# Kernel tuning notes

Measured on AMD Instinct MI355X. Metric: run time of the kernel, lower is better.

Reference implementation:

```python
import jax, jax.numpy as jnp
import numpy as np

ROPE_BASE = 10000.0
NUM_HEADS = 16

def _rotate_half(x):
    d = x.shape[-1] // 2
    return jnp.concatenate([-x[..., d:], x[..., :d]], axis=-1)

def setup_inputs() -> dict:
    key = jax.random.key(0)
    ks = jax.random.split(key, 5)
    b, s, d = 1, 2048, 2048
    scale = 1.0 / np.sqrt(d)
    return {
        "hidden_states": jax.random.normal(ks[0], (b, s, d), jnp.float32),
        "wq": jax.random.normal(ks[1], (d, d), jnp.float32) * scale,
        "wk": jax.random.normal(ks[2], (d, d), jnp.float32) * scale,
        "wv": jax.random.normal(ks[3], (d, d), jnp.float32) * scale,
        "wo": jax.random.normal(ks[4], (d, d), jnp.float32) * scale,
        "position_ids": jnp.broadcast_to(jnp.arange(s, dtype=jnp.int32), (b, s)),
    }

def reference(hidden_states, wq, wk, wv, wo, position_ids):
    b, s, d = hidden_states.shape
    h = NUM_HEADS
    dh = d // h
    # q/k/v projections (torch Linear: y = x @ W^T), split heads -> bhsd
    def proj(w):
        return jnp.einsum('bsd,ed->bse', hidden_states, w).reshape(b, s, h, dh).transpose(0, 2, 1, 3)
    q, k, v = proj(wq), proj(wk), proj(wv)
    # rotary embedding (LLaMA style): freqs over half dim, duplicated
    inv_freq = 1.0 / (ROPE_BASE ** (jnp.arange(0, dh, 2, dtype=jnp.float32) / dh))
    t = jnp.arange(s, dtype=jnp.float32)
    freqs = jnp.einsum('s,f->sf', t, inv_freq)              # [s, dh/2]
    emb = jnp.concatenate([freqs, freqs], axis=-1)          # [s, dh]
    cos = jnp.cos(emb)[position_ids][:, None, :, :]         # [b,1,s,dh]
    sin = jnp.sin(emb)[position_ids][:, None, :, :]
    q = q * cos + _rotate_half(q) * sin
    k = k * cos + _rotate_half(k) * sin
    # full (non-causal) scaled dot-product attention, as in the SDPA fast path
    scores = jnp.einsum('bhqd,bhkd->bhqk', q, k) / jnp.sqrt(jnp.float32(dh))
    attn = jax.nn.softmax(scores, axis=-1)
    out = jnp.einsum('bhqk,bhkd->bhqd', attn, v)            # [b,h,s,dh]
    out = out.transpose(0, 2, 1, 3).reshape(b, s, d)
    return jnp.einsum('bsd,ed->bse', out, wo)
```

## Files before the change

### kernel.cpp

```cpp
#include <hip/hip_runtime.h>

typedef unsigned short ushort_t;
typedef unsigned int uint32;
typedef __attribute__((ext_vector_type(8))) short short8;
typedef __attribute__((ext_vector_type(4))) float f32x4;
typedef __attribute__((ext_vector_type(2))) uint32 u32x2;

#define LDS_LOAD16(gptr, lptr)                                                             \
  __builtin_amdgcn_global_load_lds((const __attribute__((address_space(1))) uint32*)(gptr),\
                                   (__attribute__((address_space(3))) uint32*)(lptr),      \
                                   16, 0, 0)

__device__ __forceinline__ ushort_t f2b(float f) {
  uint32 u = __builtin_bit_cast(uint32, f);
  u += 0x7fffu + ((u >> 16) & 1u);
  return (ushort_t)(u >> 16);
}
__device__ __forceinline__ uint32 pk2(float a, float b) {
  return (uint32)f2b(a) | ((uint32)f2b(b) << 16);
}
__device__ __forceinline__ int swz8(int r) { return (r ^ (r >> 3)) & 7; }

constexpr size_t E = (size_t)2048 * 2048;

__global__ __launch_bounds__(256) void k_cvt5(const float* __restrict__ a0, const float* __restrict__ a1,
                                              const float* __restrict__ a2, const float* __restrict__ a3,
                                              const float* __restrict__ a4, ushort_t* __restrict__ out) {
  const float* srcs[5] = {a0, a1, a2, a3, a4};
  const float* s = srcs[blockIdx.y];
  size_t i = ((size_t)blockIdx.x * 256 + threadIdx.x) * 4;
  float4 v = *(const float4*)(s + i);
  ushort4 o;
  o.x = f2b(v.x); o.y = f2b(v.y); o.z = f2b(v.z); o.w = f2b(v.w);
  *(ushort4*)(out + (size_t)blockIdx.y * E + i) = o;
}

__global__ __launch_bounds__(256) void k_gemm_qkv(const ushort_t* __restrict__ A,
                                                  const ushort_t* __restrict__ B0,
                                                  const ushort_t* __restrict__ B1,
                                                  const ushort_t* __restrict__ B2,
                                                  ushort_t* __restrict__ Qm,
                                                  ushort_t* __restrict__ Km,
                                                  ushort_t* __restrict__ Vt,
                                                  const int* __restrict__ pos) {
  __shared__ ushort_t As[128 * 64];
  __shared__ ushort_t Bs[128 * 64];
  const int tid = threadIdx.x;
  const int lane = tid & 63, wave = tid >> 6;
  const int quad = lane >> 4, l16 = lane & 15;
  const int wm = wave >> 1, wn = wave & 1;
  const int z = blockIdx.z;
  const ushort_t* Bp = (z == 0) ? B0 : (z == 1) ? B1 : B2;
  const size_t row0 = (size_t)blockIdx.y * 128, col0 = (size_t)blockIdx.x * 128;

  int g[4];
#pragma unroll
  for (int j = 0; j < 4; ++j) g[j] = (j & 1) + ((j >> 1) << 2) + wn * 2;

  f32x4 zero = {0.f, 0.f, 0.f, 0.f};
  f32x4 acc[4][4];
#pragma unroll
  for (int i = 0; i < 4; ++i)
#pragma unroll
    for (int j = 0; j < 4; ++j) acc[i][j] = zero;

  for (int kt = 0; kt < 32; ++kt) {
#pragma unroll
    for (int j2 = 0; j2 < 4; ++j2) {
      int c = tid + 256 * j2;
      int r = c >> 3, p = c & 7;
      int sc = (p ^ swz8(r)) * 8;
      LDS_LOAD16(A + (row0 + r) * 2048 + kt * 64 + sc, &As[c * 8]);
      LDS_LOAD16(Bp + (col0 + r) * 2048 + kt * 64 + sc, &Bs[c * 8]);
    }
    __syncthreads();
    short8 a[4][2], b[4][2];
#pragma unroll
    for (int i = 0; i < 4; ++i) {
      int ra = wm * 64 + i * 16 + l16;
#pragma unroll
      for (int kk = 0; kk < 2; ++kk)
        a[i][kk] = *(const short8*)&As[(ra * 8 + ((kk * 4 + quad) ^ swz8(ra))) * 8];
    }
#pragma unroll
    for (int j = 0; j < 4; ++j) {
      int rb = g[j] * 16 + l16;
#pragma unroll
      for (int kk = 0; kk < 2; ++kk)
        b[j][kk] = *(const short8*)&Bs[(rb * 8 + ((kk * 4 + quad) ^ swz8(rb))) * 8];
    }
#pragma unroll
    for (int kk = 0; kk < 2; ++kk)
#pragma unroll
      for (int i = 0; i < 4; ++i)
#pragma unroll
        for (int j = 0; j < 4; ++j)
          acc[i][j] = __builtin_amdgcn_mfma_f32_16x16x32_bf16(a[i][kk], b[j][kk], acc[i][j], 0, 0, 0);
    __syncthreads();
  }

  if (z < 2) {
    ushort_t* C = z ? Km : Qm;
    const float mul = z ? 1.0f : 0.08838834764831845f;
#pragma unroll
    for (int i = 0; i < 4; ++i)
#pragma unroll
      for (int r = 0; r < 4; ++r) {
        size_t row = row0 + wm * 64 + i * 16 + quad * 4 + r;
        float pt = (float)pos[row];
        size_t rowoff = row * 2048 + col0;
#pragma unroll
        for (int j = 0; j < 2; ++j) {
          int f = g[j] * 16 + l16;
          float ang = pt * __expf(-0.14391156831212787f * (float)f);
          float sn, cs;
          __sincosf(ang, &sn, &cs);
          cs *= mul; sn *= mul;
          float q0 = acc[i][j][r], q1 = acc[i][j + 2][r];
          C[rowoff + f]      = f2b(q0 * cs - q1 * sn);
          C[rowoff + f + 64] = f2b(q1 * cs + q0 * sn);
        }
      }
  } else {
#pragma unroll
    for (int i = 0; i < 4; ++i)
#pragma unroll
      for (int j = 0; j < 4; ++j) {
        size_t col = col0 + g[j] * 16 + l16;
        size_t rowb = row0 + wm * 64 + i * 16 + quad * 4;
        ushort4 ov;
        ov.x = f2b(acc[i][j][0]); ov.y = f2b(acc[i][j][1]);
        ov.z = f2b(acc[i][j][2]); ov.w = f2b(acc[i][j][3]);
        *(ushort4*)&Vt[col * 2048 + rowb] = ov;
      }
  }
}

__global__ __launch_bounds__(256, 2) void k_attn(const ushort_t* __restrict__ Q,
                                                 const ushort_t* __restrict__ Kg,
                                                 const ushort_t* __restrict__ Vt,
                                                 ushort_t* __restrict__ O) {
  __shared__ uint32 smem[9216 + 256];
  ushort_t* Qs  = (ushort_t*)smem;
  uint32*   Pbf = smem + 4096;
  float*    Lred = (float*)(smem + 9216);
  float*    Rbuf = (float*)smem;

  const int tid = threadIdx.x;
  const int lane = tid & 63, wave = tid >> 6;
  const int quad = lane >> 4, l16 = lane & 15;
  const int bid = blockIdx.x;
  const int head = ((bid & 7) << 1) + ((bid >> 3) >> 5);
  const int qt = (bid >> 3) & 31;

#pragma unroll
  for (int j = 0; j < 4; ++j) {
    int s = tid + 256 * j;
    int r = s >> 4, p = s & 15;
    LDS_LOAD16(Q + (size_t)(qt * 64 + r) * 2048 + head * 128 + ((p ^ (r & 15)) * 8), &Qs[s * 8]);
  }
  __syncthreads();

  f32x4 zero = {0.f, 0.f, 0.f, 0.f};
  f32x4 oacc[4][8];
#pragma unroll
  for (int qg = 0; qg < 4; ++qg)
#pragma unroll
    for (int ns = 0; ns < 8; ++ns) oacc[qg][ns] = zero;
  float l_acc[4] = {0.f, 0.f, 0.f, 0.f};

  const ushort_t* Kbase = Kg + (size_t)head * 128;
  const ushort_t* Vbase = Vt + (size_t)head * 128 * 2048;
  uint32* pw = Pbf + wave * 1280;

  for (int it = 0; it < 16; ++it) {
    const int kb = it * 128 + wave * 32;

    short8 kf[2][4];
#pragma unroll
    for (int kg = 0; kg < 2; ++kg)
#pragma unroll
      for (int kk = 0; kk < 4; ++kk)
        kf[kg][kk] = *(const short8*)&Kbase[(size_t)(kb + kg * 16 + l16) * 2048 + kk * 32 + quad * 8];

#pragma unroll
    for (int qg = 0; qg < 4; ++qg) {
      short8 qa[4];
#pragma unroll
      for (int kk = 0; kk < 4; ++kk)
        qa[kk] = *(const short8*)&Qs[((qg * 16 + l16) * 16 + ((kk * 4 + quad) ^ l16)) * 8];
      f32x4 s0 = zero, s1 = zero;
#pragma unroll
      for (int kk = 0; kk < 4; ++kk) {
        s0 = __builtin_amdgcn_mfma_f32_16x16x32_bf16(kf[0][kk], qa[kk], s0, 0, 0, 0);
        s1 = __builtin_amdgcn_mfma_f32_16x16x32_bf16(kf[1][kk], qa[kk], s1, 0, 0, 0);
      }
      float p00 = __expf(s0[0]), p01 = __expf(s0[1]);
      float p02 = __expf(s0[2]), p03 = __expf(s0[3]);
      float p10 = __expf(s1[0]), p11 = __expf(s1[1]);
      float p12 = __expf(s1[2]), p13 = __expf(s1[3]);
      l_acc[qg] += ((p00 + p01) + (p02 + p03)) + ((p10 + p11) + (p12 + p13));
      u32x2 w0, w1;
      w0[0] = pk2(p00, p01); w0[1] = pk2(p02, p03);
      w1[0] = pk2(p10, p11); w1[1] = pk2(p12, p13);
      int off = (qg * 16 + l16) * 20 + quad * 2;
      *(u32x2*)&pw[off]     = w0;
      *(u32x2*)&pw[off + 8] = w1;
    }

    short8 pb[4];
#pragma unroll
    for (int qg = 0; qg < 4; ++qg)
      pb[qg] = *(const short8*)&pw[(qg * 16 + l16) * 20 + quad * 4];

#pragma unroll
    for (int ns = 0; ns < 8; ++ns) {
      const short8 vf = *(const short8*)&Vbase[(size_t)(ns * 16 + l16) * 2048 + kb + quad * 8];
#pragma unroll
      for (int qg = 0; qg < 4; ++qg)
        oacc[qg][ns] = __builtin_amdgcn_mfma_f32_16x16x32_bf16(vf, pb[qg], oacc[qg][ns], 0, 0, 0);
    }
  }

#pragma unroll
  for (int qg = 0; qg < 4; ++qg) {
    float l = l_acc[qg];
    l += __shfl_xor(l, 16, 64);
    l += __shfl_xor(l, 32, 64);
    l_acc[qg] = l;
  }
  if (quad == 0) {
#pragma unroll
    for (int qg = 0; qg < 4; ++qg) Lred[wave * 64 + qg * 16 + l16] = l_acc[qg];
  }

  const int tq = tid >> 4;
  const int td = (tid & 15) * 8;
  for (int qg = 0; qg < 4; ++qg) {
    __syncthreads();
#pragma unroll
    for (int ns = 0; ns < 8; ++ns)
      *(f32x4*)&Rbuf[(wave * 16 + l16) * 132 + ns * 16 + quad * 4] = oacc[qg][ns];
    __syncthreads();
    float lt = Lred[qg * 16 + tq] + Lred[64 + qg * 16 + tq] +
               Lred[128 + qg * 16 + tq] + Lred[192 + qg * 16 + tq];
    float inv = 1.0f / lt;
    f32x4 sA = zero, sB = zero;
#pragma unroll
    for (int w = 0; w < 4; ++w) {
      sA += *(const f32x4*)&Rbuf[(w * 16 + tq) * 132 + td];
      sB += *(const f32x4*)&Rbuf[(w * 16 + tq) * 132 + td + 4];
    }
    ushort4 o1, o2;
    o1.x = f2b(sA[0] * inv); o1.y = f2b(sA[1] * inv);
    o1.z = f2b(sA[2] * inv); o1.w = f2b(sA[3] * inv);
    o2.x = f2b(sB[0] * inv); o2.y = f2b(sB[1] * inv);
    o2.z = f2b(sB[2] * inv); o2.w = f2b(sB[3] * inv);
    size_t orow = (size_t)(qt * 64 + qg * 16 + tq) * 2048 + head * 128 + td;
    *(ushort4*)&O[orow] = o1;
    *(ushort4*)&O[orow + 4] = o2;
  }
}

__global__ __launch_bounds__(256) void k_gemm_wo_sk(const ushort_t* __restrict__ A,
                                                    const ushort_t* __restrict__ B,
                                                    float* __restrict__ P) {
  __shared__ ushort_t As[128 * 64];
  __shared__ ushort_t Bs[128 * 64];
  const int tid = threadIdx.x;
  const int lane = tid & 63, wave = tid >> 6;
  const int quad = lane >> 4, l16 = lane & 15;
  const int wm = wave >> 1, wn = wave & 1;
  const size_t row0 = (size_t)blockIdx.y * 128, col0 = (size_t)blockIdx.x * 128;
  const int k0 = blockIdx.z * 1024;
  float* Pz = P + (size_t)blockIdx.z * E;

  f32x4 zero = {0.f, 0.f, 0.f, 0.f};
  f32x4 acc[4][4];
#pragma unroll
  for (int i = 0; i < 4; ++i)
#pragma unroll
    for (int j = 0; j < 4; ++j) acc[i][j] = zero;

  for (int kt = 0; kt < 16; ++kt) {
#pragma unroll
    for (int j2 = 0; j2 < 4; ++j2) {
      int c = tid + 256 * j2;
      int r = c >> 3, p = c & 7;
      int sc = (p ^ swz8(r)) * 8;
      LDS_LOAD16(A + (row0 + r) * 2048 + k0 + kt * 64 + sc, &As[c * 8]);
      LDS_LOAD16(B + (col0 + r) * 2048 + k0 + kt * 64 + sc, &Bs[c * 8]);
    }
    __syncthreads();
    short8 a[4][2], b[4][2];
#pragma unroll
    for (int i = 0; i < 4; ++i) {
      int ra = wm * 64 + i * 16 + l16;
#pragma unroll
      for (int kk = 0; kk < 2; ++kk)
        a[i][kk] = *(const short8*)&As[(ra * 8 + ((kk * 4 + quad) ^ swz8(ra))) * 8];
    }
#pragma unroll
    for (int j = 0; j < 4; ++j) {
      int rb = wn * 64 + j * 16 + l16;
#pragma unroll
      for (int kk = 0; kk < 2; ++kk)
        b[j][kk] = *(const short8*)&Bs[(rb * 8 + ((kk * 4 + quad) ^ swz8(rb))) * 8];
    }
#pragma unroll
    for (int kk = 0; kk < 2; ++kk)
#pragma unroll
      for (int i = 0; i < 4; ++i)
#pragma unroll
        for (int j = 0; j < 4; ++j)
          acc[i][j] = __builtin_amdgcn_mfma_f32_16x16x32_bf16(a[i][kk], b[j][kk], acc[i][j], 0, 0, 0);
    __syncthreads();
  }

#pragma unroll
  for (int i = 0; i < 4; ++i)
#pragma unroll
    for (int j = 0; j < 4; ++j)
#pragma unroll
      for (int r = 0; r < 4; ++r) {
        size_t row = row0 + wm * 64 + i * 16 + quad * 4 + r;
        size_t col = col0 + wn * 64 + j * 16 + l16;
        Pz[row * 2048 + col] = acc[i][j][r];
      }
}

__global__ __launch_bounds__(256) void k_red(const float* __restrict__ P, float* __restrict__ out) {
  size_t i = ((size_t)blockIdx.x * 256 + threadIdx.x) * 4;
  f32x4 a = *(const f32x4*)(P + i);
  f32x4 b = *(const f32x4*)(P + E + i);
  *(f32x4*)(out + i) = a + b;
}

extern "C" void kernel_launch(void* const* d_in, const int* in_sizes, int n_in,
                              void* d_out, int out_size, void* d_ws, size_t ws_size,
                              hipStream_t stream) {
  const float* X  = (const float*)d_in[0];
  const float* wq = (const float*)d_in[1];
  const float* wk = (const float*)d_in[2];
  const float* wv = (const float*)d_in[3];
  const float* wo = (const float*)d_in[4];
  const int*  pos = (const int*)d_in[5];
  float* out = (float*)d_out;

  if (ws_size < 9 * E * sizeof(ushort_t)) return;

  ushort_t* Xb  = (ushort_t*)d_ws;
  ushort_t* Wqb = Xb + E;
  ushort_t* Wkb = Xb + 2 * E;
  ushort_t* Wvb = Xb + 3 * E;
  ushort_t* Wob = Xb + 4 * E;
  ushort_t* Qm  = Xb + 5 * E;
  ushort_t* Km  = Xb + 6 * E;
  ushort_t* Vtm = Xb + 7 * E;
  ushort_t* Om  = Xb + 8 * E;
  float* Pf = (float*)Xb;

  dim3 b256(256);
  k_cvt5<<<dim3(4096, 5), b256, 0, stream>>>(X, wq, wk, wv, wo, Xb);
  k_gemm_qkv<<<dim3(16, 16, 3), b256, 0, stream>>>(Xb, Wqb, Wkb, Wvb, Qm, Km, Vtm, pos);
  k_attn<<<512, b256, 0, stream>>>(Qm, Km, Vtm, Om);
  k_gemm_wo_sk<<<dim3(16, 16, 2), b256, 0, stream>>>(Om, Wob, Pf);
  k_red<<<4096, b256, 0, stream>>>(Pf, out);
}
```

Measured before the change: 318.8 us.

## Triple-buffer LDS in QKV and Wo GEMMs with async prefetch two tiles ahead

Result: faster. 298.1 us (-6.5%).

```diff
diff --git a/kernel.cpp b/kernel.cpp
--- a/kernel.cpp
+++ b/kernel.cpp
@@ -19,7 +19,6 @@
 __device__ __forceinline__ uint32 pk2(float a, float b) {
   return (uint32)f2b(a) | ((uint32)f2b(b) << 16);
 }
-__device__ __forceinline__ int swz8(int r) { return (r ^ (r >> 3)) & 7; }
 
 constexpr size_t E = (size_t)2048 * 2048;
 
@@ -35,16 +34,31 @@
   *(ushort4*)(out + (size_t)blockIdx.y * E + i) = o;
 }
 
-__global__ __launch_bounds__(256) void k_gemm_qkv(const ushort_t* __restrict__ A,
-                                                  const ushort_t* __restrict__ B0,
-                                                  const ushort_t* __restrict__ B1,
-                                                  const ushort_t* __restrict__ B2,
-                                                  ushort_t* __restrict__ Qm,
-                                                  ushort_t* __restrict__ Km,
-                                                  ushort_t* __restrict__ Vt,
-                                                  const int* __restrict__ pos) {
-  __shared__ ushort_t As[128 * 64];
-  __shared__ ushort_t Bs[128 * 64];
+
+#define SWZ3(r) (((r) >> 1) & 3)
+
+#define STG32(srcA, srcB, dA, dB, ktile)                                        \
+  do {                                                                          \
+    const int koff_ = (ktile) * 32;                                             \
+    _Pragma("unroll") for (int j2_ = 0; j2_ < 2; ++j2_) {                       \
+      int c_ = tid + 256 * j2_;                                                 \
+      int r_ = c_ >> 2, p_ = c_ & 3;                                            \
+      int sc_ = (p_ ^ SWZ3(r_)) * 8;                                            \
+      LDS_LOAD16((srcA) + (row0 + r_) * 2048 + koff_ + sc_, &(dA)[c_ * 8]);     \
+      LDS_LOAD16((srcB) + (col0 + r_) * 2048 + koff_ + sc_, &(dB)[c_ * 8]);     \
+    }                                                                           \
+  } while (0)
+
+__global__ __launch_bounds__(256, 3) void k_gemm_qkv(const ushort_t* __restrict__ A,
+                                                     const ushort_t* __restrict__ B0,
+                                                     const ushort_t* __restrict__ B1,
+                                                     const ushort_t* __restrict__ B2,
+                                                     ushort_t* __restrict__ Qm,
+                                                     ushort_t* __restrict__ Km,
+                                                     ushort_t* __restrict__ Vt,
+                                                     const int* __restrict__ pos) {
+  __shared__ ushort_t As[3][128 * 32];
+  __shared__ ushort_t Bs[3][128 * 32];
   const int tid = threadIdx.x;
   const int lane = tid & 63, wave = tid >> 6;
   const int quad = lane >> 4, l16 = lane & 15;
@@ -64,40 +78,42 @@
 #pragma unroll
     for (int j = 0; j < 4; ++j) acc[i][j] = zero;
 
-  for (int kt = 0; kt < 32; ++kt) {
-#pragma unroll
-    for (int j2 = 0; j2 < 4; ++j2) {
-      int c = tid + 256 * j2;
-      int r = c >> 3, p = c & 7;
-      int sc = (p ^ swz8(r)) * 8;
-      LDS_LOAD16(A + (row0 + r) * 2048 + kt * 64 + sc, &As[c * 8]);
-      LDS_LOAD16(Bp + (col0 + r) * 2048 + kt * 64 + sc, &Bs[c * 8]);
-    }
-    __syncthreads();
-    short8 a[4][2], b[4][2];
-#pragma unroll
-    for (int i = 0; i < 4; ++i) {
-      int ra = wm * 64 + i * 16 + l16;
-#pragma unroll
-      for (int kk = 0; kk < 2; ++kk)
-        a[i][kk] = *(const short8*)&As[(ra * 8 + ((kk * 4 + quad) ^ swz8(ra))) * 8];
-    }
-#pragma unroll
-    for (int j = 0; j < 4; ++j) {
-      int rb = g[j] * 16 + l16;
-#pragma unroll
-      for (int kk = 0; kk < 2; ++kk)
-        b[j][kk] = *(const short8*)&Bs[(rb * 8 + ((kk * 4 + quad) ^ swz8(rb))) * 8];
-    }
-#pragma unroll
-    for (int kk = 0; kk < 2; ++kk)
-#pragma unroll
-      for (int i = 0; i < 4; ++i)
-#pragma unroll
-        for (int j = 0; j < 4; ++j)
-          acc[i][j] = __builtin_amdgcn_mfma_f32_16x16x32_bf16(a[i][kk], b[j][kk], acc[i][j], 0, 0, 0);
-    __syncthreads();
-  }
+#define QKV_FRAGS(CUR)                                                          \
+    short8 a_[4], b_[4];                                                        \
+    _Pragma("unroll") for (int i_ = 0; i_ < 4; ++i_) {                          \
+      int ra_ = wm * 64 + i_ * 16 + l16;                                        \
+      a_[i_] = *(const short8*)&As[CUR][(ra_ * 4 + (quad ^ SWZ3(ra_))) * 8];    \
+    }                                                                           \
+    _Pragma("unroll") for (int j_ = 0; j_ < 4; ++j_) {                          \
+      int rb_ = g[j_] * 16 + l16;                                               \
+      b_[j_] = *(const short8*)&Bs[CUR][(rb_ * 4 + (quad ^ SWZ3(rb_))) * 8];    \
+    }                                                                           \
+    _Pragma("unroll") for (int i_ = 0; i_ < 4; ++i_)                            \
+      _Pragma("unroll") for (int j_ = 0; j_ < 4; ++j_)                          \
+        acc[i_][j_] = __builtin_amdgcn_mfma_f32_16x16x32_bf16(a_[i_], b_[j_], acc[i_][j_], 0, 0, 0);
+
+#define QKV_BODY(T, CUR, STG, SEN, VM)                                          \
+  do {                                                                          \
+    if (SEN) STG32(A, Bp, As[STG], Bs[STG], (T) + 2);                           \
+    QKV_FRAGS(CUR)                                                              \
+    asm volatile("s_waitcnt " VM ::: "memory");                                 \
+    __builtin_amdgcn_s_barrier();                                               \
+  } while (0)
+
+  STG32(A, Bp, As[0], Bs[0], 0);
+  STG32(A, Bp, As[1], Bs[1], 1);
+  asm volatile("s_waitcnt vmcnt(4)" ::: "memory");
+  __builtin_amdgcn_s_barrier();
+
+  for (int tt = 0; tt < 60; tt += 3) {
+    QKV_BODY(tt + 0, 0, 2, 1, "vmcnt(4)");
+    QKV_BODY(tt + 1, 1, 0, 1, "vmcnt(4)");
+    QKV_BODY(tt + 2, 2, 1, 1, "vmcnt(4)");
+  }
+  QKV_BODY(60, 0, 2, 1, "vmcnt(4)");
+  QKV_BODY(61, 1, 0, 1, "vmcnt(4)");
+  QKV_BODY(62, 2, 1, 0, "vmcnt(0)");
+  { QKV_FRAGS(0) }
 
   if (z < 2) {
     ushort_t* C = z ? Km : Qm;
@@ -262,11 +278,11 @@
   }
 }
 
-__global__ __launch_bounds__(256) void k_gemm_wo_sk(const ushort_t* __restrict__ A,
-                                                    const ushort_t* __restrict__ B,
-                                                    float* __restrict__ P) {
-  __shared__ ushort_t As[128 * 64];
-  __shared__ ushort_t Bs[128 * 64];
+__global__ __launch_bounds__(256, 3) void k_gemm_wo_sk(const ushort_t* __restrict__ A,
+                                                       const ushort_t* __restrict__ B,
+                                                       float* __restrict__ P) {
+  __shared__ ushort_t As[3][128 * 32];
+  __shared__ ushort_t Bs[3][128 * 32];
   const int tid = threadIdx.x;
   const int lane = tid & 63, wave = tid >> 6;
   const int quad = lane >> 4, l16 = lane & 15;
@@ -274,6 +290,8 @@
   const size_t row0 = (size_t)blockIdx.y * 128, col0 = (size_t)blockIdx.x * 128;
   const int k0 = blockIdx.z * 1024;
   float* Pz = P + (size_t)blockIdx.z * E;
+  const ushort_t* Ak = A + k0;
+  const ushort_t* Bk = B + k0;
 
   f32x4 zero = {0.f, 0.f, 0.f, 0.f};
   f32x4 acc[4][4];
@@ -282,40 +300,43 @@
 #pragma unroll
     for (int j = 0; j < 4; ++j) acc[i][j] = zero;
 
-  for (int kt = 0; kt < 16; ++kt) {
-#pragma unroll
-    for (int j2 = 0; j2 < 4; ++j2) {
-      int c = tid + 256 * j2;
-      int r = c >> 3, p = c & 7;
-      int sc = (p ^ swz8(r)) * 8;
-      LDS_LOAD16(A + (row0 + r) * 2048 + k0 + kt * 64 + sc, &As[c * 8]);
-      LDS_LOAD16(B + (col0 + r) * 2048 + k0 + kt * 64 + sc, &Bs[c * 8]);
-    }
-    __syncthreads();
-    short8 a[4][2], b[4][2];
-#pragma unroll
-    for (int i = 0; i < 4; ++i) {
-      int ra = wm * 64 + i * 16 + l16;
-#pragma unroll
-      for (int kk = 0; kk < 2; ++kk)
-        a[i][kk] = *(const short8*)&As[(ra * 8 + ((kk * 4 + quad) ^ swz8(ra))) * 8];
-    }
-#pragma unroll
-    for (int j = 0; j < 4; ++j) {
-      int rb = wn * 64 + j * 16 + l16;
-#pragma unroll
-      for (int kk = 0; kk < 2; ++kk)
-        b[j][kk] = *(const short8*)&Bs[(rb * 8 + ((kk * 4 + quad) ^ swz8(rb))) * 8];
-    }
-#pragma unroll
-    for (int kk = 0; kk < 2; ++kk)
-#pragma unroll
-      for (int i = 0; i < 4; ++i)
-#pragma unroll
-        for (int j = 0; j < 4; ++j)
-          acc[i][j] = __builtin_amdgcn_mfma_f32_16x16x32_bf16(a[i][kk], b[j][kk], acc[i][j], 0, 0, 0);
-    __syncthreads();
-  }
+#define WO_FRAGS(CUR)                                                           \
+    short8 a_[4], b_[4];                                                        \
+    _Pragma("unroll") for (int i_ = 0; i_ < 4; ++i_) {                          \
+      int ra_ = wm * 64 + i_ * 16 + l16;                                        \
+      a_[i_] = *(const short8*)&As[CUR][(ra_ * 4 + (quad ^ SWZ3(ra_))) * 8];    \
+    }                                                                           \
+    _Pragma("unroll") for (int j_ = 0; j_ < 4; ++j_) {                          \
+      int rb_ = wn * 64 + j_ * 16 + l16;                                        \
+      b_[j_] = *(const short8*)&Bs[CUR][(rb_ * 4 + (quad ^ SWZ3(rb_))) * 8];    \
+    }                                                                           \
+    _Pragma("unroll") for (int i_ = 0; i_ < 4; ++i_)                            \
+      _Pragma("unroll") for (int j_ = 0; j_ < 4; ++j_)                          \
+        acc[i_][j_] = __builtin_amdgcn_mfma_f32_16x16x32_bf16(a_[i_], b_[j_], acc[i_][j_], 0, 0, 0);
+
+#define WO_BODY(T, CUR, STG, SEN, VM)                                           \
+  do {                                                                          \
+    if (SEN) STG32(Ak, Bk, As[STG], Bs[STG], (T) + 2);                          \
+    WO_FRAGS(CUR)                                                               \
+    asm volatile("s_waitcnt " VM ::: "memory");                                 \
+    __builtin_amdgcn_s_barrier();                                               \
+  } while (0)
+
+  STG32(Ak, Bk, As[0], Bs[0], 0);
+  STG32(Ak, Bk, As[1], Bs[1], 1);
+  asm volatile("s_waitcnt vmcnt(4)" ::: "memory");
+  __builtin_amdgcn_s_barrier();
+
+  for (int tt = 0; tt < 27; tt += 3) {
+    WO_BODY(tt + 0, 0, 2, 1, "vmcnt(4)");
+    WO_BODY(tt + 1, 1, 0, 1, "vmcnt(4)");
+    WO_BODY(tt + 2, 2, 1, 1, "vmcnt(4)");
+  }
+  WO_BODY(27, 0, 2, 1, "vmcnt(4)");
+  WO_BODY(28, 1, 0, 1, "vmcnt(4)");
+  WO_BODY(29, 2, 1, 1, "vmcnt(4)");
+  WO_BODY(30, 0, 2, 0, "vmcnt(0)");
+  { WO_FRAGS(1) }
 
 #pragma unroll
   for (int i = 0; i < 4; ++i)
```
